# Kernel tuning notes

Measured on AMD Instinct MI355X. Metric: run time of the kernel, lower is better.

Reference implementation:

```python
import jax, jax.numpy as jnp
import numpy as np

B, S, E = 2, 2048, 2048
H, D = 16, 128  # num_attention_heads, head_dim = hidden_size // num_heads


def rotate_half(x):
    x1 = x[..., : x.shape[-1] // 2]
    x2 = x[..., x.shape[-1] // 2 :]
    return jnp.concatenate((-x2, x1), axis=-1)


def setup_inputs() -> dict:
    key = jax.random.key(0)
    ks = jax.random.split(key, 7)
    return {
        "hidden_states": jax.random.normal(ks[0], (B, S, E), dtype=jnp.float32),
        "cos": jax.random.uniform(ks[1], (1, 1, S, D), dtype=jnp.float32),
        "sin": jax.random.uniform(ks[2], (1, 1, S, D), dtype=jnp.float32),
        "wq": jax.random.normal(ks[3], (E, H * D), dtype=jnp.float32) / np.sqrt(E),
        "wk": jax.random.normal(ks[4], (E, H * D), dtype=jnp.float32) / np.sqrt(E),
        "wv": jax.random.normal(ks[5], (E, H * D), dtype=jnp.float32) / np.sqrt(E),
        "wo": jax.random.normal(ks[6], (H * D, E), dtype=jnp.float32) / np.sqrt(H * D),
    }


def reference(hidden_states, cos, sin, wq, wk, wv, wo):
    # QKV projections (no bias, per attention_bias=False)
    q = (hidden_states @ wq).reshape(B, S, H, D).transpose(0, 2, 1, 3)  # bhsd
    k = (hidden_states @ wk).reshape(B, S, H, D).transpose(0, 2, 1, 3)
    v = (hidden_states @ wv).reshape(B, S, H, D).transpose(0, 2, 1, 3)
    # RoPE (applied after the head transpose, as in the original)
    q = q * cos + rotate_half(q) * sin
    k = k * cos + rotate_half(k) * sin
    # NOTE: original forward never applies self.scaling and uses no causal mask.
    scores = jnp.einsum("bhqd,bhkd->bhqk", q, k)
    attn = jax.nn.softmax(scores.astype(jnp.float32), axis=-1)
    out = jnp.einsum("bhqk,bhkd->bhqd", attn, v)
    out = out.transpose(0, 2, 1, 3).reshape(B, S, H * D)
    return out @ wo
```

## Files before the change

kernel.cpp:

```cpp
#include <hip/hip_runtime.h>
#include <stdint.h>

typedef _Float16 f16;
typedef _Float16 half8 __attribute__((ext_vector_type(8)));
typedef _Float16 half4 __attribute__((ext_vector_type(4)));
typedef __fp16 fp16x2 __attribute__((ext_vector_type(2)));
typedef float f32x4 __attribute__((ext_vector_type(4)));
typedef float f32x16 __attribute__((ext_vector_type(16)));
typedef uint32_t u32x4 __attribute__((ext_vector_type(4)));

static constexpr int Bsz = 2, S = 2048, E = 2048, H = 16, D = 128;
static constexpr int M = Bsz * S;
static constexpr int N_QKV = 3 * H * D;
static constexpr int HD = H * D;

__device__ __forceinline__ void gload_lds16(const void* gp, void* lp) {
  __builtin_amdgcn_global_load_lds(
      (const __attribute__((address_space(1))) uint32_t*)(uintptr_t)gp,
      (__attribute__((address_space(3))) uint32_t*)(uint32_t)(uintptr_t)lp,
      16, 0, 0);
}

__device__ __forceinline__ uint32_t pkrtz(float a, float b) {
  fp16x2 r = __builtin_amdgcn_cvt_pkrtz(a, b);
  return __builtin_bit_cast(uint32_t, r);
}

__global__ void cast_f32_f16(const float* __restrict__ in, f16* __restrict__ out) {
  size_t i = (size_t)(blockIdx.x * 256 + threadIdx.x) * 8;
  float4 a = *(const float4*)&in[i];
  float4 b = *(const float4*)&in[i + 4];
  half8 h;
  h[0] = (f16)a.x; h[1] = (f16)a.y; h[2] = (f16)a.z; h[3] = (f16)a.w;
  h[4] = (f16)b.x; h[5] = (f16)b.y; h[6] = (f16)b.z; h[7] = (f16)b.w;
  *(half8*)&out[i] = h;
}

__global__ void transpose_cast(const float* __restrict__ wq, const float* __restrict__ wk,
                               const float* __restrict__ wv, const float* __restrict__ wo,
                               f16* __restrict__ wt, f16* __restrict__ wot) {
  __shared__ float tile[32][33];
  int z = blockIdx.z;
  const float* src = (z == 0) ? wq : (z == 1) ? wk : (z == 2) ? wv : wo;
  f16* dst = (z == 3) ? wot : wt + (size_t)z * E * HD;
  int bx = blockIdx.x * 32, by = blockIdx.y * 32;
  int tx = threadIdx.x, ty = threadIdx.y;
#pragma unroll
  for (int r = 0; r < 4; ++r)
    tile[ty + r * 8][tx] = src[(size_t)(by + ty + r * 8) * 2048 + bx + tx];
  __syncthreads();
#pragma unroll
  for (int r = 0; r < 4; ++r)
    dst[(size_t)(bx + ty + r * 8) * 2048 + by + tx] = (f16)tile[tx][ty + r * 8];
}

__global__ __launch_bounds__(256, 4) void qkv_fused(const f16* __restrict__ A,
                                                    const f16* __restrict__ Bt,
                                                    const float* __restrict__ cosb,
                                                    const float* __restrict__ sinb,
                                                    f16* __restrict__ Qb,
                                                    f16* __restrict__ Kb,
                                                    f16* __restrict__ VtG) {
  __shared__ f16 As[4096];
  __shared__ f16 Bs[4096];
  const int Kk = E;
  const int t = threadIdx.x, l = t & 63;
  const int wm = (t >> 7) & 1, wn = (t >> 6) & 1;
  const int lr = l & 15, g = l >> 4;
  int bid = blockIdx.x;
  int wg = (bid & 7) * 192 + (bid >> 3);
  const int bn = wg / 32, bm = wg % 32;
  const int srow = t >> 2;
  const int scol = (((t & 3) ^ (srow & 3)) * 8);
  const size_t abase = (size_t)(bm * 128 + srow) * Kk;
  const size_t bbase = (size_t)(bn * 128 + srow) * Kk;
  const int bt = bn >> 4;
  const int h = bn & 15;
  const int b = bm >> 4;
  const int bh = b * 16 + h;
  const int sblk = (bm & 15) * 128;
  f32x4 acc[4][4] = {};

  if (bt < 2) {
    for (int k0 = 0; k0 < Kk; k0 += 32) {
      __syncthreads();
      gload_lds16(&A[abase + k0 + scol], &As[t * 8]);
      gload_lds16(&A[abase + (size_t)64 * Kk + k0 + scol], &As[2048 + t * 8]);
      gload_lds16(&Bt[bbase + k0 + scol], &Bs[t * 8]);
      gload_lds16(&Bt[bbase + (size_t)64 * Kk + k0 + scol], &Bs[2048 + t * 8]);
      __syncthreads();
      half8 af[4], bf[4];
#pragma unroll
      for (int i = 0; i < 4; ++i) {
        int ra = wm * 64 + i * 16 + lr;
        af[i] = *(const half8*)&As[ra * 32 + ((g ^ (ra & 3)) * 8)];
      }
#pragma unroll
      for (int j = 0; j < 4; ++j) {
        int rb = wn * 32 + (j & 1) * 16 + (j >> 1) * 64 + lr;
        bf[j] = *(const half8*)&Bs[rb * 32 + ((g ^ (rb & 3)) * 8)];
      }
#pragma unroll
      for (int i = 0; i < 4; ++i)
#pragma unroll
        for (int j = 0; j < 4; ++j)
          acc[i][j] = __builtin_amdgcn_mfma_f32_16x16x32_f16(bf[j], af[i], acc[i][j], 0, 0, 0);
    }
    f16* Dst = (bt == 0) ? Qb : Kb;
#pragma unroll
    for (int i = 0; i < 4; ++i) {
      const int s = sblk + wm * 64 + i * 16 + lr;
      const size_t obase = ((size_t)bh * S + s) * D;
      const size_t cbase = (size_t)s * D;
#pragma unroll
      for (int j = 0; j < 2; ++j) {
        const int dlo = wn * 32 + j * 16 + g * 4;
        float4 cl = *(const float4*)&cosb[cbase + dlo];
        float4 ch = *(const float4*)&cosb[cbase + dlo + 64];
        float4 sl = *(const float4*)&sinb[cbase + dlo];
        float4 sh = *(const float4*)&sinb[cbase + dlo + 64];
        float cla[4] = {cl.x, cl.y, cl.z, cl.w}, cha[4] = {ch.x, ch.y, ch.z, ch.w};
        float sla[4] = {sl.x, sl.y, sl.z, sl.w}, sha[4] = {sh.x, sh.y, sh.z, sh.w};
        half4 olo, ohi;
#pragma unroll
        for (int r = 0; r < 4; ++r) {
          float xl = acc[i][j][r], xh = acc[i][j + 2][r];
          olo[r] = (f16)(xl * cla[r] - xh * sla[r]);
          ohi[r] = (f16)(xh * cha[r] + xl * sha[r]);
        }
        *(half4*)&Dst[obase + dlo] = olo;
        *(half4*)&Dst[obase + dlo + 64] = ohi;
      }
    }
  } else {
    for (int k0 = 0; k0 < Kk; k0 += 32) {
      __syncthreads();
      gload_lds16(&A[abase + k0 + scol], &As[t * 8]);
      gload_lds16(&A[abase + (size_t)64 * Kk + k0 + scol], &As[2048 + t * 8]);
      gload_lds16(&Bt[bbase + k0 + scol], &Bs[t * 8]);
      gload_lds16(&Bt[bbase + (size_t)64 * Kk + k0 + scol], &Bs[2048 + t * 8]);
      __syncthreads();
      half8 af[4], bf[4];
#pragma unroll
      for (int i = 0; i < 4; ++i) {
        int ra = wm * 64 + i * 16 + lr;
        int rb = wn * 64 + i * 16 + lr;
        af[i] = *(const half8*)&As[ra * 32 + ((g ^ (ra & 3)) * 8)];
        bf[i] = *(const half8*)&Bs[rb * 32 + ((g ^ (rb & 3)) * 8)];
      }
#pragma unroll
      for (int i = 0; i < 4; ++i)
#pragma unroll
        for (int j = 0; j < 4; ++j)
          acc[i][j] = __builtin_amdgcn_mfma_f32_16x16x32_f16(af[i], bf[j], acc[i][j], 0, 0, 0);
    }
#pragma unroll
    for (int j = 0; j < 4; ++j) {
      int d = wn * 64 + j * 16 + lr;
      size_t rowb = ((size_t)bh * D + d) * S;
#pragma unroll
      for (int i = 0; i < 4; ++i) {
        int s0 = sblk + wm * 64 + i * 16 + g * 4;
        half4 h4;
#pragma unroll
        for (int r = 0; r < 4; ++r) h4[r] = (f16)acc[i][j][r];
        *(half4*)&VtG[rowb + s0] = h4;
      }
    }
  }
}

template <typename OutT>
__global__ __launch_bounds__(256, 4) void gemm_bt(const f16* __restrict__ A,
                                                  const f16* __restrict__ Bt,
                                                  OutT* __restrict__ C,
                                                  int Mm, int Nn, int Kk) {
  __shared__ f16 As[128 * 32];
  __shared__ f16 Bs[128 * 32];
  const int t = threadIdx.x, l = t & 63;
  const int wm = (t >> 7) & 1, wn = (t >> 6) & 1;
  const int bm = blockIdx.x, bn = blockIdx.y;
  const int lr = l & 15, g = l >> 4;
  const int srow = t >> 2;
  const int schunk = t & 3;
  const int scol = ((schunk ^ (srow & 3)) * 8);
  const size_t abase = (size_t)(bm * 128 + srow) * Kk;
  const size_t bbase = (size_t)(bn * 128 + srow) * Kk;
  f32x4 acc[4][4] = {};
  for (int k0 = 0; k0 < Kk; k0 += 32) {
    __syncthreads();
    gload_lds16(&A[abase + k0 + scol], &As[t * 8]);
    gload_lds16(&A[abase + (size_t)64 * Kk + k0 + scol], &As[2048 + t * 8]);
    gload_lds16(&Bt[bbase + k0 + scol], &Bs[t * 8]);
    gload_lds16(&Bt[bbase + (size_t)64 * Kk + k0 + scol], &Bs[2048 + t * 8]);
    __syncthreads();
    half8 af[4], bf[4];
#pragma unroll
    for (int i = 0; i < 4; ++i) {
      int ra = wm * 64 + i * 16 + lr;
      int rb = wn * 64 + i * 16 + lr;
      af[i] = *(const half8*)&As[ra * 32 + ((g ^ (ra & 3)) * 8)];
      bf[i] = *(const half8*)&Bs[rb * 32 + ((g ^ (rb & 3)) * 8)];
    }
#pragma unroll
    for (int i = 0; i < 4; ++i)
#pragma unroll
      for (int j = 0; j < 4; ++j)
        acc[i][j] = __builtin_amdgcn_mfma_f32_16x16x32_f16(af[i], bf[j], acc[i][j], 0, 0, 0);
  }
#pragma unroll
  for (int i = 0; i < 4; ++i)
#pragma unroll
    for (int j = 0; j < 4; ++j) {
      int row = bm * 128 + wm * 64 + i * 16 + g * 4;
      int col = bn * 128 + wn * 64 + j * 16 + lr;
#pragma unroll
      for (int r = 0; r < 4; ++r)
        C[(size_t)(row + r) * Nn + col] = (OutT)acc[i][j][r];
    }
}

__device__ __forceinline__ void stage_kv(const f16* __restrict__ Kg, const f16* __restrict__ Vg,
                                         f16* KsB, f16* VsB, int t, int kv) {
#pragma unroll
  for (int rnd = 0; rnd < 4; ++rnd) {
    int row = rnd * 16 + (t >> 4);
    int c = t & 15;
    gload_lds16(&Kg[(size_t)(kv + row) * D + ((c ^ (row & 7)) * 8)], &KsB[rnd * 2048 + t * 8]);
  }
#pragma unroll
  for (int rnd = 0; rnd < 4; ++rnd) {
    int row = rnd * 32 + (t >> 3);
    int c = t & 7;
    gload_lds16(&Vg[(size_t)row * S + kv + ((c ^ (row & 7)) * 8)], &VsB[rnd * 2048 + t * 8]);
  }
}

__global__ __launch_bounds__(256, 2) void flash_attn2(const f16* __restrict__ Q,
                                                      const f16* __restrict__ K,
                                                      const f16* __restrict__ Vt,
                                                      f16* __restrict__ O) {
  __shared__ f16 lds[2][16384];
  const int t = threadIdx.x, l = t & 63, w = t >> 6;
  const int c = l & 31, hi = l >> 5;
  int bid = blockIdx.x;
  bid = (bid & 7) * 64 + (bid >> 3);
  const int bh = bid >> 4, qt = bid & 15;
  const size_t baseQ = (size_t)bh * S * D;
  const f16* Kg = K + baseQ;
  const f16* Vg = Vt + (size_t)bh * D * S;
  const int q0 = qt * 128 + w * 32;
  half8 qf[8];
#pragma unroll
  for (int dc = 0; dc < 8; ++dc)
    qf[dc] = *(const half8*)&Q[baseQ + (size_t)(q0 + c) * D + dc * 16 + hi * 8];
  f32x16 o[4] = {};
  float m = -3.0e38f, ssum = 0.f;

  stage_kv(Kg, Vg, &lds[0][0], &lds[0][8192], t, 0);
  __syncthreads();

  for (int it = 0; it < S / 64; ++it) {
    const int cur = it & 1;
    const f16* KsB = &lds[cur][0];
    const f16* VsB = &lds[cur][8192];
    if (it + 1 < S / 64) stage_kv(Kg, Vg, &lds[cur ^ 1][0], &lds[cur ^ 1][8192], t, (it + 1) * 64);

    f32x16 s0 = {}, s1 = {};
    __builtin_amdgcn_s_setprio(1);
#pragma unroll
    for (int dc = 0; dc < 8; ++dc) {
      const int r0 = c, r1 = 32 + c;
      half8 kf0 = *(const half8*)&KsB[r0 * 128 + (((2 * dc + hi) ^ (r0 & 7)) * 8)];
      half8 kf1 = *(const half8*)&KsB[r1 * 128 + (((2 * dc + hi) ^ (r1 & 7)) * 8)];
      s0 = __builtin_amdgcn_mfma_f32_32x32x16_f16(kf0, qf[dc], s0, 0, 0, 0);
      s1 = __builtin_amdgcn_mfma_f32_32x32x16_f16(kf1, qf[dc], s1, 0, 0, 0);
    }
    __builtin_amdgcn_s_setprio(0);

    float tm = s0[0];
#pragma unroll
    for (int r = 1; r < 16; ++r) tm = fmaxf(tm, s0[r]);
#pragma unroll
    for (int r = 0; r < 16; ++r) tm = fmaxf(tm, s1[r]);
    tm = fmaxf(tm, __shfl_xor(tm, 32));
    float mn = fmaxf(m, tm);
    float corr = __expf(m - mn);
    m = mn;
    float ts = 0.f;
#pragma unroll
    for (int r = 0; r < 16; ++r) { s0[r] = __expf(s0[r] - mn); ts += s0[r]; }
#pragma unroll
    for (int r = 0; r < 16; ++r) { s1[r] = __expf(s1[r] - mn); ts += s1[r]; }
    ts += __shfl_xor(ts, 32);
    ssum = ssum * corr + ts;
#pragma unroll
    for (int dt = 0; dt < 4; ++dt)
#pragma unroll
      for (int r = 0; r < 16; ++r) o[dt][r] *= corr;

    half8 pf[4];
#pragma unroll
    for (int ks = 0; ks < 4; ++ks) {
      const int B0 = 2 * (ks & 1), B1 = B0 + 1;
      uint32_t X0, X1, Y0, Y1;
      if (ks < 2) {
        X0 = pkrtz(s0[4 * B0 + 0], s0[4 * B0 + 1]);
        X1 = pkrtz(s0[4 * B0 + 2], s0[4 * B0 + 3]);
        Y0 = pkrtz(s0[4 * B1 + 0], s0[4 * B1 + 1]);
        Y1 = pkrtz(s0[4 * B1 + 2], s0[4 * B1 + 3]);
      } else {
        X0 = pkrtz(s1[4 * B0 + 0], s1[4 * B0 + 1]);
        X1 = pkrtz(s1[4 * B0 + 2], s1[4 * B0 + 3]);
        Y0 = pkrtz(s1[4 * B1 + 0], s1[4 * B1 + 1]);
        Y1 = pkrtz(s1[4 * B1 + 2], s1[4 * B1 + 3]);
      }
      asm volatile("v_permlane32_swap_b32 %0, %1" : "+v"(X0), "+v"(Y0));
      asm volatile("v_permlane32_swap_b32 %0, %1" : "+v"(X1), "+v"(Y1));
      u32x4 pw; pw[0] = X0; pw[1] = X1; pw[2] = Y0; pw[3] = Y1;
      pf[ks] = __builtin_bit_cast(half8, pw);
    }

    __builtin_amdgcn_s_setprio(1);
#pragma unroll
    for (int dt = 0; dt < 4; ++dt) {
      const int row = dt * 32 + c;
#pragma unroll
      for (int ks = 0; ks < 4; ++ks) {
        half8 vf = *(const half8*)&VsB[row * 64 + (((2 * ks + hi) ^ (row & 7)) * 8)];
        o[dt] = __builtin_amdgcn_mfma_f32_32x32x16_f16(vf, pf[ks], o[dt], 0, 0, 0);
      }
    }
    __builtin_amdgcn_s_setprio(0);
    __syncthreads();
  }

  const float inv = 1.f / ssum;
  const int b = bh >> 4, h = bh & 15;
  const size_t orow = ((size_t)(b * S + q0 + c)) * HD + h * D;
#pragma unroll
  for (int dt = 0; dt < 4; ++dt)
#pragma unroll
    for (int b2 = 0; b2 < 4; ++b2) {
      half4 h4;
#pragma unroll
      for (int a = 0; a < 4; ++a) h4[a] = (f16)(o[dt][4 * b2 + a] * inv);
      *(half4*)&O[orow + dt * 32 + 8 * b2 + 4 * hi] = h4;
    }
}

extern "C" void kernel_launch(void* const* d_in, const int* in_sizes, int n_in,
                              void* d_out, int out_size, void* d_ws, size_t ws_size,
                              hipStream_t stream) {
  (void)in_sizes; (void)n_in; (void)out_size; (void)ws_size;
  const float* hs = (const float*)d_in[0];
  const float* cosb = (const float*)d_in[1];
  const float* sinb = (const float*)d_in[2];
  const float* wq = (const float*)d_in[3];
  const float* wk = (const float*)d_in[4];
  const float* wv = (const float*)d_in[5];
  const float* wo = (const float*)d_in[6];
  float* out = (float*)d_out;
  char* ws = (char*)d_ws;
  f16* hs16 = (f16*)(ws);
  f16* attn = (f16*)(ws);
  f16* wt   = (f16*)(ws + (16u << 20));
  f16* wot  = (f16*)(ws + (40u << 20));
  f16* Qb   = (f16*)(ws + (48u << 20));
  f16* Kb   = (f16*)(ws + (64u << 20));
  f16* VtG  = (f16*)(ws + (80u << 20));

  cast_f32_f16<<<dim3(4096), dim3(256), 0, stream>>>(hs, hs16);
  transpose_cast<<<dim3(64, 64, 4), dim3(32, 8), 0, stream>>>(wq, wk, wv, wo, wt, wot);
  qkv_fused<<<dim3(1536), dim3(256), 0, stream>>>(hs16, wt, cosb, sinb, Qb, Kb, VtG);
  flash_attn2<<<dim3(512), dim3(256), 0, stream>>>(Qb, Kb, VtG, attn);
  gemm_bt<float><<<dim3(32, 16), dim3(256), 0, stream>>>(attn, wot, out, M, E, HD);
}
```

Before: 304.3 us.

## Rewrite QKV and output GEMMs as 8-wave pipelined kernels; lazy softmax rescale

Replaces the 256-thread 128x128 GEMM kernels for the QKV projection and the output projection with 512-thread kernels that compute 256x128 tiles. They double-buffer LDS with async global-to-LDS loads staged two k-steps ahead and gate them with explicit vmcnt waits and barriers. The aim is to overlap memory loads with MFMA work and raise data reuse per block. Separately, flash attention now skips the running-max update and output rescale unless the new tile max exceeds the old max by more than 8 across the wavefront. This trades exact max tracking for fewer exp and multiply ops, at some overflow and precision risk.

```diff
diff --git a/kernel.cpp b/kernel.cpp
--- a/kernel.cpp
+++ b/kernel.cpp
@@ -54,58 +54,102 @@
     dst[(size_t)(bx + ty + r * 8) * 2048 + by + tx] = (f16)tile[tx][ty + r * 8];
 }
 
-__global__ __launch_bounds__(256, 4) void qkv_fused(const f16* __restrict__ A,
-                                                    const f16* __restrict__ Bt,
-                                                    const float* __restrict__ cosb,
-                                                    const float* __restrict__ sinb,
-                                                    f16* __restrict__ Qb,
-                                                    f16* __restrict__ Kb,
-                                                    f16* __restrict__ VtG) {
-  __shared__ f16 As[4096];
-  __shared__ f16 Bs[4096];
+#define ABUF(b_, kh_) ((b_) * 16384 + (kh_) * 8192)
+#define BBUF(b_) (32768 + (b_) * 8192)
+#define STAGE_A(T_, kh_)                                                     \
+  do {                                                                       \
+    int ko_ = (T_) * 64 + (kh_) * 32;                                        \
+    int bb_ = (T_) & 1;                                                      \
+    gload_lds16(Abase + ko_ + ca0, &lds[ABUF(bb_, kh_) + t * 8]);            \
+    gload_lds16(Abase + ko_ + ca1, &lds[ABUF(bb_, kh_) + 4096 + t * 8]);     \
+  } while (0)
+#define STAGE_B(T_)                                                          \
+  do {                                                                       \
+    int ko_ = (T_) * 64;                                                     \
+    int bb_ = (T_) & 1;                                                      \
+    gload_lds16(Br0 + ko_, &lds[BBUF(bb_) + t * 8]);                         \
+    gload_lds16(Br1 + ko_, &lds[BBUF(bb_) + 4096 + t * 8]);                  \
+  } while (0)
+#define LDA2(mq_, kh_)                                                       \
+  _Pragma("unroll") for (int i2 = 0; i2 < 2; ++i2) {                         \
+    int ra = wm * 64 + ((mq_)*2 + i2) * 16 + lr;                             \
+    int s_ = g ^ ((ra >> 2) & 3);                                            \
+    af[i2] = *(const half8*)&lds[ABUF(cb, kh_) + (s_ >> 1) * 4096 + ra * 16 + (s_ & 1) * 8]; \
+  }
+#define LDB_GEN(kh_, RB_)                                                    \
+  _Pragma("unroll") for (int j = 0; j < 4; ++j) {                            \
+    int rb = (RB_);                                                          \
+    bf[j] = *(const half8*)&lds[BBUF(cb) + rb * 64 + ((((kh_)*4) + g) ^ (rb & 7)) * 8]; \
+  }
+#define MM8(mq_, SWAP_)                                                      \
+  __builtin_amdgcn_s_setprio(1);                                             \
+  _Pragma("unroll") for (int i2 = 0; i2 < 2; ++i2)                           \
+  _Pragma("unroll") for (int j = 0; j < 4; ++j)                              \
+      acc[(mq_)*2 + i2][j] = (SWAP_)                                         \
+          ? __builtin_amdgcn_mfma_f32_16x16x32_f16(bf[j], af[i2], acc[(mq_)*2 + i2][j], 0, 0, 0) \
+          : __builtin_amdgcn_mfma_f32_16x16x32_f16(af[i2], bf[j], acc[(mq_)*2 + i2][j], 0, 0, 0); \
+  __builtin_amdgcn_s_setprio(0);
+#define BAR() __builtin_amdgcn_s_barrier()
+#define VM6() asm volatile("s_waitcnt vmcnt(6)" ::: "memory")
+#define VM4() asm volatile("s_waitcnt vmcnt(4)" ::: "memory")
+#define VM0() asm volatile("s_waitcnt vmcnt(0)" ::: "memory")
+
+#define KLOOP(RB_, SWAP_)                                                    \
+  for (int T = 0; T < 32; ++T) {                                             \
+    const int cb = T & 1;                                                    \
+    half8 af[2], bf[4];                                                      \
+    LDB_GEN(0, RB_); LDA2(0, 0);                                             \
+    if (T + 1 < 32) STAGE_A(T + 1, 1);                                       \
+    BAR(); MM8(0, SWAP_); BAR();                                             \
+    LDA2(1, 0);                                                              \
+    if (T >= 29) { VM0(); } else { VM6(); }                                  \
+    BAR(); MM8(1, SWAP_); BAR();                                             \
+    LDB_GEN(1, RB_); LDA2(0, 1);                                             \
+    if (T + 2 < 32) STAGE_A(T + 2, 0);                                       \
+    BAR(); MM8(0, SWAP_); BAR();                                             \
+    LDA2(1, 1);                                                              \
+    if (T + 2 < 32) STAGE_B(T + 2);                                          \
+    if (T >= 29) { VM0(); } else { VM6(); }                                  \
+    BAR(); MM8(1, SWAP_); BAR();                                             \
+  }
+
+__global__ __launch_bounds__(512, 1) void qkv8(const f16* __restrict__ A,
+                                               const f16* __restrict__ Bt,
+                                               const float* __restrict__ cosb,
+                                               const float* __restrict__ sinb,
+                                               f16* __restrict__ Qb,
+                                               f16* __restrict__ Kb,
+                                               f16* __restrict__ VtG) {
+  __shared__ f16 lds[49152];
   const int Kk = E;
-  const int t = threadIdx.x, l = t & 63;
-  const int wm = (t >> 7) & 1, wn = (t >> 6) & 1;
+  const int t = threadIdx.x, l = t & 63, wid = t >> 6;
+  const int wm = wid >> 1, wn = wid & 1;
   const int lr = l & 15, g = l >> 4;
-  int bid = blockIdx.x;
-  int wg = (bid & 7) * 192 + (bid >> 3);
-  const int bn = wg / 32, bm = wg % 32;
-  const int srow = t >> 2;
-  const int scol = (((t & 3) ^ (srow & 3)) * 8);
-  const size_t abase = (size_t)(bm * 128 + srow) * Kk;
-  const size_t bbase = (size_t)(bn * 128 + srow) * Kk;
-  const int bt = bn >> 4;
-  const int h = bn & 15;
-  const int b = bm >> 4;
-  const int bh = b * 16 + h;
-  const int sblk = (bm & 15) * 128;
+  const int bid = blockIdx.x;
+  const int ii = bid >> 3;
+  const int bm = (bid & 7) * 2 + (ii & 1);
+  const int bn = ii >> 1;
+  const int arow = t >> 1, ah = t & 1;
+  const int fa = (arow >> 2) & 3;
+  const int ca0 = (ah ^ fa) * 8;
+  const int ca1 = ((2 | ah) ^ fa) * 8;
+  const f16* Abase = A + (size_t)(bm * 256 + arow) * Kk;
+  const int brl = t >> 3, bc = t & 7;
+  const int cbx = (bc ^ (brl & 7)) * 8;
+  const f16* Br0 = Bt + (size_t)(bn * 128 + brl) * Kk + cbx;
+  const f16* Br1 = Bt + (size_t)(bn * 128 + 64 + brl) * Kk + cbx;
+  const int bt = bn >> 4, h = bn & 15;
+  const int bh = (bm >> 3) * 16 + h;
+  const int sblk = (bm & 7) * 256;
+
   f32x4 acc[4][4] = {};
+  STAGE_A(0, 0); STAGE_A(0, 1); STAGE_B(0);
+  STAGE_A(1, 0); STAGE_B(1);
+  VM4();
+  BAR();
 
   if (bt < 2) {
-    for (int k0 = 0; k0 < Kk; k0 += 32) {
-      __syncthreads();
-      gload_lds16(&A[abase + k0 + scol], &As[t * 8]);
-      gload_lds16(&A[abase + (size_t)64 * Kk + k0 + scol], &As[2048 + t * 8]);
-      gload_lds16(&Bt[bbase + k0 + scol], &Bs[t * 8]);
-      gload_lds16(&Bt[bbase + (size_t)64 * Kk + k0 + scol], &Bs[2048 + t * 8]);
-      __syncthreads();
-      half8 af[4], bf[4];
-#pragma unroll
-      for (int i = 0; i < 4; ++i) {
-        int ra = wm * 64 + i * 16 + lr;
-        af[i] = *(const half8*)&As[ra * 32 + ((g ^ (ra & 3)) * 8)];
-      }
-#pragma unroll
-      for (int j = 0; j < 4; ++j) {
-        int rb = wn * 32 + (j & 1) * 16 + (j >> 1) * 64 + lr;
-        bf[j] = *(const half8*)&Bs[rb * 32 + ((g ^ (rb & 3)) * 8)];
-      }
-#pragma unroll
-      for (int i = 0; i < 4; ++i)
-#pragma unroll
-        for (int j = 0; j < 4; ++j)
-          acc[i][j] = __builtin_amdgcn_mfma_f32_16x16x32_f16(bf[j], af[i], acc[i][j], 0, 0, 0);
-    }
+    KLOOP(wn * 32 + (j & 1) * 16 + (j >> 1) * 64 + lr, true)
     f16* Dst = (bt == 0) ? Qb : Kb;
 #pragma unroll
     for (int i = 0; i < 4; ++i) {
@@ -133,27 +177,7 @@
       }
     }
   } else {
-    for (int k0 = 0; k0 < Kk; k0 += 32) {
-      __syncthreads();
-      gload_lds16(&A[abase + k0 + scol], &As[t * 8]);
-      gload_lds16(&A[abase + (size_t)64 * Kk + k0 + scol], &As[2048 + t * 8]);
-      gload_lds16(&Bt[bbase + k0 + scol], &Bs[t * 8]);
-      gload_lds16(&Bt[bbase + (size_t)64 * Kk + k0 + scol], &Bs[2048 + t * 8]);
-      __syncthreads();
-      half8 af[4], bf[4];
-#pragma unroll
-      for (int i = 0; i < 4; ++i) {
-        int ra = wm * 64 + i * 16 + lr;
-        int rb = wn * 64 + i * 16 + lr;
-        af[i] = *(const half8*)&As[ra * 32 + ((g ^ (ra & 3)) * 8)];
-        bf[i] = *(const half8*)&Bs[rb * 32 + ((g ^ (rb & 3)) * 8)];
-      }
-#pragma unroll
-      for (int i = 0; i < 4; ++i)
-#pragma unroll
-        for (int j = 0; j < 4; ++j)
-          acc[i][j] = __builtin_amdgcn_mfma_f32_16x16x32_f16(af[i], bf[j], acc[i][j], 0, 0, 0);
-    }
+    KLOOP(wn * 64 + j * 16 + lr, false)
 #pragma unroll
     for (int j = 0; j < 4; ++j) {
       int d = wn * 64 + j * 16 + lr;
@@ -170,53 +194,44 @@
   }
 }
 
-template <typename OutT>
-__global__ __launch_bounds__(256, 4) void gemm_bt(const f16* __restrict__ A,
-                                                  const f16* __restrict__ Bt,
-                                                  OutT* __restrict__ C,
-                                                  int Mm, int Nn, int Kk) {
-  __shared__ f16 As[128 * 32];
-  __shared__ f16 Bs[128 * 32];
-  const int t = threadIdx.x, l = t & 63;
-  const int wm = (t >> 7) & 1, wn = (t >> 6) & 1;
-  const int bm = blockIdx.x, bn = blockIdx.y;
+__global__ __launch_bounds__(512, 1) void gemm8o(const f16* __restrict__ A,
+                                                 const f16* __restrict__ Bt,
+                                                 float* __restrict__ C) {
+  __shared__ f16 lds[49152];
+  const int Kk = HD;
+  const int t = threadIdx.x, l = t & 63, wid = t >> 6;
+  const int wm = wid >> 1, wn = wid & 1;
   const int lr = l & 15, g = l >> 4;
-  const int srow = t >> 2;
-  const int schunk = t & 3;
-  const int scol = ((schunk ^ (srow & 3)) * 8);
-  const size_t abase = (size_t)(bm * 128 + srow) * Kk;
-  const size_t bbase = (size_t)(bn * 128 + srow) * Kk;
+  const int bid = blockIdx.x;
+  const int ii = bid >> 3;
+  const int bm = (bid & 7) * 2 + (ii & 1);
+  const int bn = ii >> 1;
+  const int arow = t >> 1, ah = t & 1;
+  const int fa = (arow >> 2) & 3;
+  const int ca0 = (ah ^ fa) * 8;
+  const int ca1 = ((2 | ah) ^ fa) * 8;
+  const f16* Abase = A + (size_t)(bm * 256 + arow) * Kk;
+  const int brl = t >> 3, bc = t & 7;
+  const int cbx = (bc ^ (brl & 7)) * 8;
+  const f16* Br0 = Bt + (size_t)(bn * 128 + brl) * Kk + cbx;
+  const f16* Br1 = Bt + (size_t)(bn * 128 + 64 + brl) * Kk + cbx;
+
   f32x4 acc[4][4] = {};
-  for (int k0 = 0; k0 < Kk; k0 += 32) {
-    __syncthreads();
-    gload_lds16(&A[abase + k0 + scol], &As[t * 8]);
-    gload_lds16(&A[abase + (size_t)64 * Kk + k0 + scol], &As[2048 + t * 8]);
-    gload_lds16(&Bt[bbase + k0 + scol], &Bs[t * 8]);
-    gload_lds16(&Bt[bbase + (size_t)64 * Kk + k0 + scol], &Bs[2048 + t * 8]);
-    __syncthreads();
-    half8 af[4], bf[4];
-#pragma unroll
-    for (int i = 0; i < 4; ++i) {
-      int ra = wm * 64 + i * 16 + lr;
-      int rb = wn * 64 + i * 16 + lr;
-      af[i] = *(const half8*)&As[ra * 32 + ((g ^ (ra & 3)) * 8)];
-      bf[i] = *(const half8*)&Bs[rb * 32 + ((g ^ (rb & 3)) * 8)];
-    }
-#pragma unroll
-    for (int i = 0; i < 4; ++i)
-#pragma unroll
-      for (int j = 0; j < 4; ++j)
-        acc[i][j] = __builtin_amdgcn_mfma_f32_16x16x32_f16(af[i], bf[j], acc[i][j], 0, 0, 0);
-  }
+  STAGE_A(0, 0); STAGE_A(0, 1); STAGE_B(0);
+  STAGE_A(1, 0); STAGE_B(1);
+  VM4();
+  BAR();
+  KLOOP(wn * 64 + j * 16 + lr, false)
+
 #pragma unroll
   for (int i = 0; i < 4; ++i)
 #pragma unroll
     for (int j = 0; j < 4; ++j) {
-      int row = bm * 128 + wm * 64 + i * 16 + g * 4;
+      int row = bm * 256 + wm * 64 + i * 16 + g * 4;
       int col = bn * 128 + wn * 64 + j * 16 + lr;
 #pragma unroll
       for (int r = 0; r < 4; ++r)
-        C[(size_t)(row + r) * Nn + col] = (OutT)acc[i][j][r];
+        C[(size_t)(row + r) * E + col] = acc[i][j][r];
     }
 }
 
@@ -284,20 +299,23 @@
 #pragma unroll
     for (int r = 0; r < 16; ++r) tm = fmaxf(tm, s1[r]);
     tm = fmaxf(tm, __shfl_xor(tm, 32));
-    float mn = fmaxf(m, tm);
-    float corr = __expf(m - mn);
-    m = mn;
+    if (!__all(tm <= m + 8.f)) {
+      float mn = fmaxf(m, tm);
+      float corr = __expf(m - mn);
+      m = mn;
+      ssum *= corr;
+#pragma unroll
+      for (int dt = 0; dt < 4; ++dt)
+#pragma unroll
+        for (int r = 0; r < 16; ++r) o[dt][r] *= corr;
+    }
     float ts = 0.f;
 #pragma unroll
-    for (int r = 0; r < 16; ++r) { s0[r] = __expf(s0[r] - mn); ts += s0[r]; }
-#pragma unroll
-    for (int r = 0; r < 16; ++r) { s1[r] = __expf(s1[r] - mn); ts += s1[r]; }
+    for (int r = 0; r < 16; ++r) { s0[r] = __expf(s0[r] - m); ts += s0[r]; }
+#pragma unroll
+    for (int r = 0; r < 16; ++r) { s1[r] = __expf(s1[r] - m); ts += s1[r]; }
     ts += __shfl_xor(ts, 32);
-    ssum = ssum * corr + ts;
-#pragma unroll
-    for (int dt = 0; dt < 4; ++dt)
-#pragma unroll
-      for (int r = 0; r < 16; ++r) o[dt][r] *= corr;
+    ssum += ts;
 
     half8 pf[4];
 #pragma unroll
@@ -372,7 +390,7 @@
 
   cast_f32_f16<<<dim3(4096), dim3(256), 0, stream>>>(hs, hs16);
   transpose_cast<<<dim3(64, 64, 4), dim3(32, 8), 0, stream>>>(wq, wk, wv, wo, wt, wot);
-  qkv_fused<<<dim3(1536), dim3(256), 0, stream>>>(hs16, wt, cosb, sinb, Qb, Kb, VtG);
+  qkv8<<<dim3(768), dim3(512), 0, stream>>>(hs16, wt, cosb, sinb, Qb, Kb, VtG);
   flash_attn2<<<dim3(512), dim3(256), 0, stream>>>(Qb, Kb, VtG, attn);
-  gemm_bt<float><<<dim3(32, 16), dim3(256), 0, stream>>>(attn, wot, out, M, E, HD);
-}
+  gemm8o<<<dim3(256), dim3(512), 0, stream>>>(attn, wot, out);
+}
```

After: 290.1 us. 1.05x faster.
